# Optimization experiments

Measured on AMD Instinct MI355X. Metric: run time of the kernel, lower is better.

Reference implementation:

```python
import jax, jax.numpy as jnp
import numpy as np

NUM_BATCHES = 8  # number of sparse-tensor batch instances


def setup_inputs() -> dict:
    key = jax.random.key(0)
    k1, k2, k3, k4 = jax.random.split(key, 4)
    N, C, R = 262144, 256, 4
    Cr = C // R
    x_feats = jax.random.normal(k1, (N, C), dtype=jnp.float32)
    batch_ids = jax.random.randint(k2, (N,), 0, NUM_BATCHES, dtype=jnp.int32)
    # MinkowskiLinear params (kaiming-ish scale)
    W1 = jax.random.normal(k3, (C, Cr), dtype=jnp.float32) * (1.0 / np.sqrt(C))
    b1 = jnp.zeros((Cr,), dtype=jnp.float32)
    W2 = jax.random.normal(k4, (Cr, C), dtype=jnp.float32) * (1.0 / np.sqrt(Cr))
    b2 = jnp.zeros((C,), dtype=jnp.float32)
    return {"x_feats": x_feats, "batch_ids": batch_ids, "W1": W1, "b1": b1, "W2": W2, "b2": b2}


def reference(x_feats, batch_ids, W1, b1, W2, b2):
    # MinkowskiGlobalPooling: per-batch average over irregular point sets -> [B, C]
    sums = jax.ops.segment_sum(x_feats, batch_ids, num_segments=NUM_BATCHES)
    counts = jax.ops.segment_sum(jnp.ones((x_feats.shape[0],), x_feats.dtype),
                                 batch_ids, num_segments=NUM_BATCHES)
    pooled = sums / jnp.maximum(counts, 1.0)[:, None]  # [B, C]
    # Squeeze-excite MLP: Linear -> ReLU -> Linear -> Sigmoid
    h = jax.nn.relu(pooled @ W1 + b1)                  # [B, C/r]
    y = jax.nn.sigmoid(h @ W2 + b2)                    # [B, C]
    # Broadcast excitation back to each sparse point and multiply
    return y[batch_ids] * x_feats                      # [N, C]
```

## Files before the change

kernel.cpp:

```cpp
#include <hip/hip_runtime.h>
#include <math.h>

#define NB 8
#define C  256
#define CR 64

#define POOL_BLOCKS  512
#define SCALE_BLOCKS 2048

typedef float vf4 __attribute__((ext_vector_type(4)));

__global__ __launch_bounds__(256) void pool_kernel(
    const float* __restrict__ x,
    const int*   __restrict__ bids,
    float*       __restrict__ partials,
    float*       __restrict__ cpart,
    int N)
{
    __shared__ float lsum[4][NB][C];
    __shared__ float lcnt[4][NB];

    const int tid  = threadIdx.x;
    const int wid  = tid >> 6;
    const int lane = tid & 63;

    vf4   acc[NB];
    float cnt[NB];
    #pragma unroll
    for (int b = 0; b < NB; ++b) { acc[b] = (vf4){0.f,0.f,0.f,0.f}; cnt[b] = 0.f; }

    const int gwave   = blockIdx.x * 4 + wid;
    const int totw    = POOL_BLOCKS * 4;
    const int ngroups = N >> 2;

    int g = gwave;
    if (g < ngroups) {
        size_t r0 = (size_t)g * 4;
        int4 bb = *((const int4*)(bids + r0));
        vf4 v0 = __builtin_nontemporal_load(((const vf4*)(x + (r0 + 0) * C)) + lane);
        vf4 v1 = __builtin_nontemporal_load(((const vf4*)(x + (r0 + 1) * C)) + lane);
        vf4 v2 = __builtin_nontemporal_load(((const vf4*)(x + (r0 + 2) * C)) + lane);
        vf4 v3 = __builtin_nontemporal_load(((const vf4*)(x + (r0 + 3) * C)) + lane);
        while (true) {
            const int gn = g + totw;
            const bool more = (gn < ngroups);
            int4 nb; vf4 n0, n1, n2, n3;
            if (more) {
                const size_t rn = (size_t)gn * 4;
                nb = *((const int4*)(bids + rn));
                n0 = __builtin_nontemporal_load(((const vf4*)(x + (rn + 0) * C)) + lane);
                n1 = __builtin_nontemporal_load(((const vf4*)(x + (rn + 1) * C)) + lane);
                n2 = __builtin_nontemporal_load(((const vf4*)(x + (rn + 2) * C)) + lane);
                n3 = __builtin_nontemporal_load(((const vf4*)(x + (rn + 3) * C)) + lane);
            }
            const int b0 = __builtin_amdgcn_readfirstlane(bb.x);
            const int b1 = __builtin_amdgcn_readfirstlane(bb.y);
            const int b2 = __builtin_amdgcn_readfirstlane(bb.z);
            const int b3 = __builtin_amdgcn_readfirstlane(bb.w);
            #pragma unroll
            for (int b = 0; b < NB; ++b) {
                const float m0 = (b0 == b) ? 1.f : 0.f;
                const float m1 = (b1 == b) ? 1.f : 0.f;
                const float m2 = (b2 == b) ? 1.f : 0.f;
                const float m3 = (b3 == b) ? 1.f : 0.f;
                acc[b] += v0 * m0;
                acc[b] += v1 * m1;
                acc[b] += v2 * m2;
                acc[b] += v3 * m3;
                cnt[b] += m0 + m1 + m2 + m3;
            }
            if (!more) break;
            bb = nb; v0 = n0; v1 = n1; v2 = n2; v3 = n3; g = gn;
        }
    }
    if (gwave == 0) {
        for (int row = ngroups * 4; row < N; ++row) {
            const int bb = __builtin_amdgcn_readfirstlane(bids[row]);
            const vf4 v = ((const vf4*)(x + (size_t)row * C))[lane];
            #pragma unroll
            for (int b = 0; b < NB; ++b) {
                const float m = (bb == b) ? 1.f : 0.f;
                acc[b] += v * m;
                cnt[b] += m;
            }
        }
    }

    #pragma unroll
    for (int b = 0; b < NB; ++b)
        ((vf4*)&lsum[wid][b][0])[lane] = acc[b];
    if (lane == 0) {
        #pragma unroll
        for (int b = 0; b < NB; ++b) lcnt[wid][b] = cnt[b];
    }
    __syncthreads();

    float* pout = partials + (size_t)blockIdx.x * (NB * C);
    for (int i = tid; i < NB * C; i += 256)
        pout[i] = lsum[0][0][i] + lsum[1][0][i] + lsum[2][0][i] + lsum[3][0][i];
    if (tid < NB)
        cpart[blockIdx.x * NB + tid] =
            lcnt[0][tid] + lcnt[1][tid] + lcnt[2][tid] + lcnt[3][tid];
}

__global__ __launch_bounds__(256) void reduce_kernel(
    const float* __restrict__ partials,
    const float* __restrict__ cpart,
    float*       __restrict__ partial2,
    float*       __restrict__ c2)
{
    const int jo  = blockIdx.x & 7;
    const int jp  = blockIdx.x >> 3;
    const int col = jo * 256 + threadIdx.x;
    const int PR  = POOL_BLOCKS / 8;

    float s = 0.f;
    #pragma unroll 8
    for (int p = 0; p < PR; ++p)
        s += partials[(size_t)(jp * PR + p) * (NB * C) + col];
    partial2[jp * (NB * C) + col] = s;

    if (jo == 0 && threadIdx.x < NB) {
        float c = 0.f;
        for (int p = 0; p < PR; ++p)
            c += cpart[(jp * PR + p) * NB + threadIdx.x];
        c2[jp * NB + threadIdx.x] = c;
    }
}

__global__ __launch_bounds__(256) void mlp_kernel(
    const float* __restrict__ partial2,
    const float* __restrict__ c2,
    const float* __restrict__ W1,
    const float* __restrict__ b1,
    const float* __restrict__ W2,
    const float* __restrict__ b2,
    float*       __restrict__ y)
{
    __shared__ float pooled[NB][C];
    __shared__ float h[NB][CR];
    __shared__ float cnts[NB];
    const int tid = threadIdx.x;

    if (tid < NB) {
        float c = 0.f;
        #pragma unroll
        for (int j = 0; j < 8; ++j) c += c2[j * NB + tid];
        cnts[tid] = fmaxf(c, 1.f);
    }
    __syncthreads();

    for (int i = tid; i < NB * C; i += 256) {
        float s = 0.f;
        #pragma unroll
        for (int j = 0; j < 8; ++j) s += partial2[j * (NB * C) + i];
        (&pooled[0][0])[i] = s / cnts[i >> 8];
    }
    __syncthreads();

    for (int o = tid; o < NB * CR; o += 256) {
        const int b = o >> 6, j = o & 63;
        float acc = b1[j];
        #pragma unroll 4
        for (int k = 0; k < C; ++k) acc = fmaf(pooled[b][k], W1[k * CR + j], acc);
        (&h[0][0])[o] = fmaxf(acc, 0.f);
    }
    __syncthreads();

    for (int o = tid; o < NB * C; o += 256) {
        const int b = o >> 8, j = o & 255;
        float acc = b2[j];
        #pragma unroll
        for (int k = 0; k < CR; ++k) acc = fmaf(h[b][k], W2[k * C + j], acc);
        y[o] = 1.f / (1.f + __expf(-acc));
    }
}

__global__ __launch_bounds__(256) void scale_kernel(
    const float* __restrict__ x,
    const int*   __restrict__ bids,
    const float* __restrict__ y,
    float*       __restrict__ out,
    int N)
{
    __shared__ float ly[NB][C];
    const int tid = threadIdx.x;
    for (int i = tid; i < NB * C; i += 256) (&ly[0][0])[i] = y[i];
    __syncthreads();

    const int wid  = tid >> 6;
    const int lane = tid & 63;
    const int gwave   = blockIdx.x * 4 + wid;
    const int totw    = SCALE_BLOCKS * 4;
    const int ngroups = N >> 2;

    int g = gwave;
    if (g < ngroups) {
        size_t r0 = (size_t)g * 4;
        int4 bb = *((const int4*)(bids + r0));
        vf4 v0 = __builtin_nontemporal_load(((const vf4*)(x + (r0 + 0) * C)) + lane);
        vf4 v1 = __builtin_nontemporal_load(((const vf4*)(x + (r0 + 1) * C)) + lane);
        vf4 v2 = __builtin_nontemporal_load(((const vf4*)(x + (r0 + 2) * C)) + lane);
        vf4 v3 = __builtin_nontemporal_load(((const vf4*)(x + (r0 + 3) * C)) + lane);
        while (true) {
            const int gn = g + totw;
            const bool more = (gn < ngroups);
            int4 nb; vf4 n0, n1, n2, n3;
            if (more) {
                const size_t rn = (size_t)gn * 4;
                nb = *((const int4*)(bids + rn));
                n0 = __builtin_nontemporal_load(((const vf4*)(x + (rn + 0) * C)) + lane);
                n1 = __builtin_nontemporal_load(((const vf4*)(x + (rn + 1) * C)) + lane);
                n2 = __builtin_nontemporal_load(((const vf4*)(x + (rn + 2) * C)) + lane);
                n3 = __builtin_nontemporal_load(((const vf4*)(x + (rn + 3) * C)) + lane);
            }
            const size_t r0c = (size_t)g * 4;
            const int b0 = __builtin_amdgcn_readfirstlane(bb.x);
            const int b1 = __builtin_amdgcn_readfirstlane(bb.y);
            const int b2 = __builtin_amdgcn_readfirstlane(bb.z);
            const int b3 = __builtin_amdgcn_readfirstlane(bb.w);
            const vf4 g0 = ((const vf4*)&ly[b0][0])[lane];
            const vf4 g1 = ((const vf4*)&ly[b1][0])[lane];
            const vf4 g2 = ((const vf4*)&ly[b2][0])[lane];
            const vf4 g3 = ((const vf4*)&ly[b3][0])[lane];
            __builtin_nontemporal_store(v0 * g0, ((vf4*)(out + (r0c + 0) * C)) + lane);
            __builtin_nontemporal_store(v1 * g1, ((vf4*)(out + (r0c + 1) * C)) + lane);
            __builtin_nontemporal_store(v2 * g2, ((vf4*)(out + (r0c + 2) * C)) + lane);
            __builtin_nontemporal_store(v3 * g3, ((vf4*)(out + (r0c + 3) * C)) + lane);
            if (!more) break;
            bb = nb; v0 = n0; v1 = n1; v2 = n2; v3 = n3; g = gn;
        }
    }
    if (gwave == 0) {
        for (int row = ngroups * 4; row < N; ++row) {
            const int bb = __builtin_amdgcn_readfirstlane(bids[row]);
            const vf4 v  = ((const vf4*)(x + (size_t)row * C))[lane];
            const vf4 gg = ((const vf4*)&ly[bb][0])[lane];
            ((vf4*)(out + (size_t)row * C))[lane] = v * gg;
        }
    }
}

extern "C" void kernel_launch(void* const* d_in, const int* in_sizes, int n_in,
                              void* d_out, int out_size, void* d_ws, size_t ws_size,
                              hipStream_t stream)
{
    const float* x    = (const float*)d_in[0];
    const int*   bids = (const int*)  d_in[1];
    const float* W1   = (const float*)d_in[2];
    const float* b1   = (const float*)d_in[3];
    const float* W2   = (const float*)d_in[4];
    const float* b2   = (const float*)d_in[5];
    float* out = (float*)d_out;

    const int N = in_sizes[1];

    float* partials = (float*)d_ws;
    float* cpart    = partials + POOL_BLOCKS * (NB * C);
    float* partial2 = cpart + POOL_BLOCKS * NB;
    float* c2       = partial2 + 8 * (NB * C);
    float* gy       = c2 + 64;

    pool_kernel  <<<POOL_BLOCKS, 256, 0, stream>>>(x, bids, partials, cpart, N);
    reduce_kernel<<<64, 256, 0, stream>>>(partials, cpart, partial2, c2);
    mlp_kernel   <<<1, 256, 0, stream>>>(partial2, c2, W1, b1, W2, b2, gy);
    scale_kernel <<<SCALE_BLOCKS, 256, 0, stream>>>(x, bids, gy, out, N);
}
```

Baseline: 163.5 us.

## Fuse partial reduction and MLP into one kernel with a grid barrier

Merges the two-level reduce kernel and the single-block MLP kernel into one 64-block kernel. Each block reduces a column slice over all pool partials, then all blocks meet at an atomic-counter grid barrier (reset by the pool kernel). After the barrier every block recomputes the first MLP layer redundantly and produces its own 32 outputs of the second layer. This removes one launch and the serial single-block MLP, but relies on all 64 blocks being co-resident for the spin barrier and repeats the W1 work in every block.

```diff
diff --git a/kernel.cpp b/kernel.cpp
--- a/kernel.cpp
+++ b/kernel.cpp
@@ -7,6 +7,7 @@
 
 #define POOL_BLOCKS  512
 #define SCALE_BLOCKS 2048
+#define RM_BLOCKS    64
 
 typedef float vf4 __attribute__((ext_vector_type(4)));
 
@@ -15,6 +16,7 @@
     const int*   __restrict__ bids,
     float*       __restrict__ partials,
     float*       __restrict__ cpart,
+    int*         __restrict__ ctl,
     int N)
 {
     __shared__ float lsum[4][NB][C];
@@ -23,6 +25,8 @@
     const int tid  = threadIdx.x;
     const int wid  = tid >> 6;
     const int lane = tid & 63;
+
+    if (blockIdx.x == 0 && tid == 0) *ctl = 0;
 
     vf4   acc[NB];
     float cnt[NB];
@@ -103,76 +107,85 @@
             lcnt[0][tid] + lcnt[1][tid] + lcnt[2][tid] + lcnt[3][tid];
 }
 
-__global__ __launch_bounds__(256) void reduce_kernel(
+__global__ __launch_bounds__(256) void reduce_mlp_kernel(
     const float* __restrict__ partials,
     const float* __restrict__ cpart,
-    float*       __restrict__ partial2,
-    float*       __restrict__ c2)
-{
-    const int jo  = blockIdx.x & 7;
-    const int jp  = blockIdx.x >> 3;
-    const int col = jo * 256 + threadIdx.x;
-    const int PR  = POOL_BLOCKS / 8;
-
-    float s = 0.f;
-    #pragma unroll 8
-    for (int p = 0; p < PR; ++p)
-        s += partials[(size_t)(jp * PR + p) * (NB * C) + col];
-    partial2[jp * (NB * C) + col] = s;
-
-    if (jo == 0 && threadIdx.x < NB) {
-        float c = 0.f;
-        for (int p = 0; p < PR; ++p)
-            c += cpart[(jp * PR + p) * NB + threadIdx.x];
-        c2[jp * NB + threadIdx.x] = c;
-    }
-}
-
-__global__ __launch_bounds__(256) void mlp_kernel(
-    const float* __restrict__ partial2,
-    const float* __restrict__ c2,
     const float* __restrict__ W1,
     const float* __restrict__ b1,
     const float* __restrict__ W2,
     const float* __restrict__ b2,
+    float*       __restrict__ gsums,
+    float*       __restrict__ gcnts,
+    int*         __restrict__ ctl,
     float*       __restrict__ y)
 {
-    __shared__ float pooled[NB][C];
-    __shared__ float h[NB][CR];
-    __shared__ float cnts[NB];
+    __shared__ float red[256];
+    __shared__ float credbuf[64];
+    __shared__ float pl[NB * C];
+    __shared__ float h[NB * CR];
+    __shared__ float cn[NB];
+
     const int tid = threadIdx.x;
-
-    if (tid < NB) {
+    const int blk = blockIdx.x;
+
+    const int col = blk * 32 + (tid & 31);
+    const int rg  = tid >> 5;
+    float s = 0.f;
+    #pragma unroll 8
+    for (int r = rg; r < POOL_BLOCKS; r += 8)
+        s += partials[(size_t)r * (NB * C) + col];
+    red[tid] = s;
+    if (blk == 0 && tid < 64) {
+        const int b = tid & 7, rs = tid >> 3;
         float c = 0.f;
-        #pragma unroll
-        for (int j = 0; j < 8; ++j) c += c2[j * NB + tid];
-        cnts[tid] = fmaxf(c, 1.f);
-    }
-    __syncthreads();
-
-    for (int i = tid; i < NB * C; i += 256) {
-        float s = 0.f;
-        #pragma unroll
-        for (int j = 0; j < 8; ++j) s += partial2[j * (NB * C) + i];
-        (&pooled[0][0])[i] = s / cnts[i >> 8];
-    }
-    __syncthreads();
-
+        for (int r = rs; r < POOL_BLOCKS; r += 8) c += cpart[r * NB + b];
+        credbuf[tid] = c;
+    }
+    __syncthreads();
+    if (rg == 0) {
+        float t = 0.f;
+        #pragma unroll
+        for (int k = 0; k < 8; ++k) t += red[k * 32 + tid];
+        gsums[blk * 32 + tid] = t;
+    }
+    if (blk == 0 && tid < NB) {
+        float t = 0.f;
+        #pragma unroll
+        for (int k = 0; k < 8; ++k) t += credbuf[k * 8 + tid];
+        gcnts[tid] = t;
+    }
+
+    __syncthreads();
+    if (tid == 0) {
+        __threadfence();
+        atomicAdd(ctl, 1);
+        while (__hip_atomic_load(ctl, __ATOMIC_RELAXED,
+                                 __HIP_MEMORY_SCOPE_AGENT) < RM_BLOCKS)
+            __builtin_amdgcn_s_sleep(8);
+        __threadfence();
+    }
+    __syncthreads();
+
+    if (tid < NB) cn[tid] = fmaxf(gcnts[tid], 1.f);
+    __syncthreads();
+    for (int i = tid; i < NB * C; i += 256)
+        pl[i] = gsums[i] / cn[i >> 8];
+    __syncthreads();
     for (int o = tid; o < NB * CR; o += 256) {
         const int b = o >> 6, j = o & 63;
-        float acc = b1[j];
+        float a = b1[j];
         #pragma unroll 4
-        for (int k = 0; k < C; ++k) acc = fmaf(pooled[b][k], W1[k * CR + j], acc);
-        (&h[0][0])[o] = fmaxf(acc, 0.f);
-    }
-    __syncthreads();
-
-    for (int o = tid; o < NB * C; o += 256) {
+        for (int k = 0; k < C; ++k) a = fmaf(pl[b * C + k], W1[k * CR + j], a);
+        h[o] = fmaxf(a, 0.f);
+    }
+    __syncthreads();
+    if (tid < 32) {
+        const int o = blk * 32 + tid;
         const int b = o >> 8, j = o & 255;
-        float acc = b2[j];
-        #pragma unroll
-        for (int k = 0; k < CR; ++k) acc = fmaf(h[b][k], W2[k * C + j], acc);
-        y[o] = 1.f / (1.f + __expf(-acc));
+        float a = b2[j];
+        #pragma unroll
+        for (int k = 0; k < CR; ++k) a = fmaf(h[b * CR + k], W2[k * C + j], a);
+        y[o] = 1.f / (1.f + __expf(-a));
     }
 }
 
@@ -257,12 +270,13 @@
 
     float* partials = (float*)d_ws;
     float* cpart    = partials + POOL_BLOCKS * (NB * C);
-    float* partial2 = cpart + POOL_BLOCKS * NB;
-    float* c2       = partial2 + 8 * (NB * C);
-    float* gy       = c2 + 64;
-
-    pool_kernel  <<<POOL_BLOCKS, 256, 0, stream>>>(x, bids, partials, cpart, N);
-    reduce_kernel<<<64, 256, 0, stream>>>(partials, cpart, partial2, c2);
-    mlp_kernel   <<<1, 256, 0, stream>>>(partial2, c2, W1, b1, W2, b2, gy);
-    scale_kernel <<<SCALE_BLOCKS, 256, 0, stream>>>(x, bids, gy, out, N);
-}
+    float* gsums    = cpart + POOL_BLOCKS * NB;
+    float* gcnts    = gsums + NB * C;
+    int*   ctl      = (int*)(gcnts + NB);
+    float* gy       = gcnts + NB + 8;
+
+    pool_kernel      <<<POOL_BLOCKS, 256, 0, stream>>>(x, bids, partials, cpart, ctl, N);
+    reduce_mlp_kernel<<<RM_BLOCKS, 256, 0, stream>>>(partials, cpart, W1, b1, W2, b2,
+                                                     gsums, gcnts, ctl, gy);
+    scale_kernel     <<<SCALE_BLOCKS, 256, 0, stream>>>(x, bids, gy, out, N);
+}
```

Result: slower. 176.4 us (+7.9%).
